# Performance work log

Measured on AMD Instinct MI355X. Metric: run time of the kernel, lower is better.

Reference implementation:

```python
import jax, jax.numpy as jnp
import numpy as np

N = 50000      # nodes
E = 800000     # edges
IN = 128       # in_dim
H = 8          # heads
C = 16         # h_dim (per-head out channels)
ED = 16        # edge_dim
G = 1000       # number of graphs
HC = H * C     # 128
EPS = 1e-16    # PyG softmax epsilon


def setup_inputs() -> dict:
    key = jax.random.key(0)
    ks = jax.random.split(key, 32)
    p = lambda i, shape: jax.random.normal(ks[i], shape, jnp.float32) * 0.1
    inp = {
        "x": jax.random.normal(ks[0], (N, IN), jnp.float32),
        "edge_index": jax.random.randint(ks[1], (2, E), 0, N),
        "edge_attr": jax.random.normal(ks[2], (E, ED), jnp.float32),
        "batch": jnp.sort(jax.random.randint(ks[3], (N,), 0, G)),
    }
    dims = [IN, HC, HC]
    for l in range(3):
        d = dims[l]
        inp[f"W{l+1}"] = p(4 + 6 * l, (d, HC))     # lin weight
        inp[f"We{l+1}"] = p(5 + 6 * l, (ED, HC))   # lin_edge weight
        inp[f"as{l+1}"] = p(6 + 6 * l, (H, C))     # att_src
        inp[f"ad{l+1}"] = p(7 + 6 * l, (H, C))     # att_dst
        inp[f"ae{l+1}"] = p(8 + 6 * l, (H, C))     # att_edge
        inp[f"b{l+1}"] = jnp.zeros((HC,), jnp.float32)
    D = 4 * HC  # cat(h1,h2,h3,h_pool_) -> 512
    inp["Wl1"] = p(22, (D, D)); inp["bl1"] = jnp.zeros((D,), jnp.float32)
    inp["Wl2"] = p(23, (D, 1)); inp["bl2"] = jnp.zeros((1,), jnp.float32)
    return inp


def gat_conv(x, src, dst, edge_attr, W, We, a_s, a_d, a_e, b):
    # x: [N, d_in] -> xs: [N, H, C]
    xs = (x @ W).reshape(-1, H, C)
    ea = (edge_attr @ We).reshape(-1, H, C)          # [E, H, C]
    al_src = jnp.sum(xs * a_s, axis=-1)              # [N, H]
    al_dst = jnp.sum(xs * a_d, axis=-1)              # [N, H]
    al_e = jnp.sum(ea * a_e, axis=-1)                # [E, H]
    alpha = al_src[src] + al_dst[dst] + al_e         # [E, H]
    alpha = jax.nn.leaky_relu(alpha, 0.2)
    amax = jax.ops.segment_max(alpha, dst, num_segments=N)
    ex = jnp.exp(alpha - amax[dst])
    denom = jax.ops.segment_sum(ex, dst, num_segments=N)
    alpha = ex / (denom[dst] + EPS)                  # softmax over in-edges of dst
    msg = xs[src] * alpha[..., None]                 # [E, H, C]
    out = jax.ops.segment_sum(msg, dst, num_segments=N)  # [N, H, C]
    return out.reshape(-1, HC) + b


def reference(x, edge_index, edge_attr, batch,
              W1, We1, as1, ad1, ae1, b1,
              W2, We2, as2, ad2, ae2, b2,
              W3, We3, as3, ad3, ae3, b3,
              Wl1, bl1, Wl2, bl2):
    src, dst = edge_index[0], edge_index[1]
    h1 = gat_conv(x, src, dst, edge_attr, W1, We1, as1, ad1, ae1, b1)
    h2 = gat_conv(h1, src, dst, edge_attr, W2, We2, as2, ad2, ae2, b2)
    h3 = gat_conv(h2, src, dst, edge_attr, W3, We3, as3, ad3, ae3, b3)
    # global_add_pool then broadcast back per node (vectorized gather,
    # replacing the original per-node python loop)
    h_pool = jax.ops.segment_sum(h3, batch, num_segments=G)   # [G, HC]
    h_pool_ = h_pool[batch]                                    # [N, HC]
    h = jnp.concatenate([h1, h2, h3, h_pool_], axis=1)         # [N, 4*HC]
    h = jax.nn.leaky_relu(h @ Wl1 + bl1, 0.01)
    return h @ Wl2 + bl2
```

## Files before the change

kernel.cpp:

```cpp
#include <hip/hip_runtime.h>

#define N_NODES 50000
#define N_EDGES 800000
#define N_GRAPH 1000
#define EPAD (N_EDGES + 8 * N_NODES)

typedef short bf16x8 __attribute__((ext_vector_type(8)));
typedef float f32x4 __attribute__((ext_vector_type(4)));

__device__ inline short f2b(float f) {
    union { float f; unsigned u; } x; x.f = f;
    unsigned r = x.u + 0x7FFF + ((x.u >> 16) & 1);
    return (short)(r >> 16);
}
__device__ inline float b2f_lo(unsigned v) {
    union { unsigned u; float f; } x; x.u = v << 16; return x.f;
}
__device__ inline float b2f_hi(unsigned v) {
    union { unsigned u; float f; } x; x.u = v & 0xFFFF0000u; return x.f;
}
__device__ inline float b2f_s(short s) {
    union { unsigned u; float f; } x; x.u = ((unsigned)(unsigned short)s) << 16; return x.f;
}
__device__ inline unsigned pack2(short lo, short hi) {
    return ((unsigned)(unsigned short)lo) | (((unsigned)(unsigned short)hi) << 16);
}

__global__ void wbt3_k(const float* __restrict__ W0, const float* __restrict__ W1,
                       const float* __restrict__ W2, short* __restrict__ wbt) {
    int l = blockIdx.x >> 6;
    const float* W = (l == 0) ? W0 : (l == 1) ? W1 : W2;
    int idx = (blockIdx.x & 63) * 256 + threadIdx.x;
    int k = idx >> 7, c = idx & 127;
    wbt[(size_t)l * 16384 + (size_t)c * 128 + k] = f2b(W[idx]);
}

__global__ void aew3_k(const float* __restrict__ We0, const float* __restrict__ ae0,
                       const float* __restrict__ We1, const float* __restrict__ ae1,
                       const float* __restrict__ We2, const float* __restrict__ ae2,
                       float* __restrict__ aeW3) {
    const float* We = (blockIdx.x == 0) ? We0 : (blockIdx.x == 1) ? We1 : We2;
    const float* ae = (blockIdx.x == 0) ? ae0 : (blockIdx.x == 1) ? ae1 : ae2;
    int t = threadIdx.x;
    int k = t >> 3, h = t & 7;
    float s = 0.f;
#pragma unroll
    for (int c = 0; c < 16; c++) s += We[k * 128 + h * 16 + c] * ae[h * 16 + c];
    aeW3[blockIdx.x * 128 + t] = s;
}

template <bool AF32>
__global__ __launch_bounds__(256) void gemm_mfma(const void* __restrict__ Aptr,
                                                 const short* __restrict__ WbT,
                                                 short* __restrict__ outb, int nrows) {
    const int tid = threadIdx.x;
    const int n0 = blockIdx.x * 64;
    const int wid = tid >> 6, lane = tid & 63;
    const int lr = lane & 15, kg = lane >> 4;
    const int wr = (wid >> 1) * 32;
    const int wc = (wid & 1) * 64;

    f32x4 acc[2][4] = {};

#pragma unroll
    for (int ks = 0; ks < 4; ks++) {
        const int k0 = ks * 32;
        bf16x8 a[2], b[4];
#pragma unroll
        for (int fm = 0; fm < 2; fm++) {
            int gr = n0 + wr + fm * 16 + lr;
            bf16x8 v = {};
            if (gr < nrows) {
                if (AF32) {
                    const float* ap = (const float*)Aptr + (size_t)gr * 128 + k0 + kg * 8;
                    float4 f0 = *(const float4*)(ap);
                    float4 f1 = *(const float4*)(ap + 4);
                    v[0] = f2b(f0.x); v[1] = f2b(f0.y); v[2] = f2b(f0.z); v[3] = f2b(f0.w);
                    v[4] = f2b(f1.x); v[5] = f2b(f1.y); v[6] = f2b(f1.z); v[7] = f2b(f1.w);
                } else {
                    v = *(const bf16x8*)((const short*)Aptr + (size_t)gr * 128 + k0 + kg * 8);
                }
            }
            a[fm] = v;
        }
#pragma unroll
        for (int fn = 0; fn < 4; fn++)
            b[fn] = *(const bf16x8*)(WbT + (size_t)(wc + fn * 16 + lr) * 128 + k0 + kg * 8);
#pragma unroll
        for (int fm = 0; fm < 2; fm++)
#pragma unroll
            for (int fn = 0; fn < 4; fn++)
                acc[fm][fn] = __builtin_amdgcn_mfma_f32_16x16x32_bf16(
                    a[fm], b[fn], acc[fm][fn], 0, 0, 0);
    }
#pragma unroll
    for (int fm = 0; fm < 2; fm++) {
#pragma unroll
        for (int r = 0; r < 4; r++) {
            int gr = n0 + wr + fm * 16 + kg * 4 + r;
            if (gr < nrows) {
#pragma unroll
                for (int fn = 0; fn < 4; fn++) {
                    int col = wc + fn * 16 + lr;
                    outb[(size_t)gr * 128 + col] = f2b(acc[fm][fn][r]);
                }
            }
        }
    }
}

__global__ void node_al(const short* __restrict__ xsb, const float* __restrict__ a_s,
                        const float* __restrict__ a_d, float* __restrict__ alsrc,
                        float* __restrict__ aldst, int n) {
    int t = blockIdx.x * blockDim.x + threadIdx.x;
    if (t >= n * 8) return;
    int node = t >> 3, h = t & 7;
    const short* xp = xsb + (size_t)node * 128 + h * 16;
    uint4 u0 = *(const uint4*)(xp);
    uint4 u1 = *(const uint4*)(xp + 8);
    unsigned w[8] = {u0.x, u0.y, u0.z, u0.w, u1.x, u1.y, u1.z, u1.w};
    float ss = 0.f, dd = 0.f;
#pragma unroll
    for (int q = 0; q < 8; q++) {
        float lo = b2f_lo(w[q]), hi = b2f_hi(w[q]);
        ss += lo * a_s[h * 16 + q * 2] + hi * a_s[h * 16 + q * 2 + 1];
        dd += lo * a_d[h * 16 + q * 2] + hi * a_d[h * 16 + q * 2 + 1];
    }
    alsrc[t] = ss;
    aldst[t] = dd;
}

__global__ void hist_k(const int* __restrict__ ei, int* __restrict__ cnt, int ne) {
    int e = blockIdx.x * blockDim.x + threadIdx.x;
    if (e < ne) atomicAdd(&cnt[ei[ne + e]], 1);
}

__global__ void scan1_k(const int* __restrict__ cnt, int* __restrict__ rowptr,
                        int* __restrict__ part, int n) {
    __shared__ int s[256];
    int tid = threadIdx.x;
    int i = blockIdx.x * 256 + tid;
    int v = (i < n) ? ((cnt[i] + 7) & ~7) : 0;
    s[tid] = v; __syncthreads();
#pragma unroll
    for (int off = 1; off < 256; off <<= 1) {
        int t = (tid >= off) ? s[tid - off] : 0;
        __syncthreads();
        s[tid] += t;
        __syncthreads();
    }
    if (i < n) rowptr[i] = s[tid] - v;
    if (tid == 255) part[blockIdx.x] = s[255];
}

__global__ void scan2_k(int* __restrict__ part, int npart) {
    __shared__ int s[256];
    int tid = threadIdx.x;
    int v = (tid < npart) ? part[tid] : 0;
    s[tid] = v; __syncthreads();
#pragma unroll
    for (int off = 1; off < 256; off <<= 1) {
        int t = (tid >= off) ? s[tid - off] : 0;
        __syncthreads();
        s[tid] += t;
        __syncthreads();
    }
    if (tid < npart) part[tid] = s[tid] - v;
}

__global__ void scan3_k(int* __restrict__ rowptr, const int* __restrict__ part,
                        const int* __restrict__ cnt, int* __restrict__ cursor, int n) {
    int i = blockIdx.x * 256 + threadIdx.x;
    if (i < n) {
        int r = rowptr[i] + part[blockIdx.x];
        rowptr[i] = r;
        cursor[i] = r;
        if (i == n - 1) rowptr[n] = r + ((cnt[i] + 7) & ~7);
    }
}

__global__ void scatter_k(const int* __restrict__ ei, const float* __restrict__ eattr,
                          int* __restrict__ cursor, int* __restrict__ csr_src,
                          short* __restrict__ eatb, int ne) {
    int e = blockIdx.x * blockDim.x + threadIdx.x;
    if (e >= ne) return;
    int d = ei[ne + e];
    int p = atomicAdd(&cursor[d], 1);
    csr_src[p] = ei[e];
    const float4* ep = (const float4*)(eattr + (size_t)e * 16);
    short* op = eatb + (size_t)p * 16;
#pragma unroll
    for (int q = 0; q < 4; q++) {
        float4 v = ep[q];
        *(short4*)(op + q * 4) = make_short4(f2b(v.x), f2b(v.y), f2b(v.z), f2b(v.w));
    }
}

__global__ void gbound_k(const int* __restrict__ batch, int* __restrict__ gb, int n, int g) {
    int i = blockIdx.x * 256 + threadIdx.x;
    if (i >= n) return;
    int b1 = batch[i];
    int b0 = (i == 0) ? -1 : batch[i - 1];
    for (int q = b0 + 1; q <= b1; q++) gb[q] = i;
    if (i == n - 1)
        for (int q = b1 + 1; q <= g; q++) gb[q] = n;
}

__global__ __launch_bounds__(256) void pools_k(const short* __restrict__ h3b,
                                               const int* __restrict__ gb,
                                               short* __restrict__ poolb) {
    __shared__ float red[128];
    int g = blockIdx.x;
    int c = threadIdx.x & 127;
    int par = threadIdx.x >> 7;
    int i0 = gb[g], i1 = gb[g + 1];
    float s = 0.f;
    for (int i = i0 + par; i < i1; i += 2) s += b2f_s(h3b[(size_t)i * 128 + c]);
    if (par == 1) red[c] = s;
    __syncthreads();
    if (par == 0) poolb[(size_t)g * 128 + c] = f2b(s + red[c]);
}

__global__ __launch_bounds__(256) void gather_k(const int* __restrict__ rowptr,
                                                const int* __restrict__ csr_src,
                                                const short* __restrict__ eatb,
                                                const float* __restrict__ aeW,
                                                const float* __restrict__ alsrc,
                                                const float* __restrict__ aldst,
                                                const short* __restrict__ xsb,
                                                const float* __restrict__ b,
                                                short* __restrict__ houtb, int n) {
    __shared__ float sAe[128];
    if (threadIdx.x < 128) sAe[threadIdx.x] = aeW[threadIdx.x];
    __syncthreads();
    int dst = blockIdx.x * 4 + (threadIdx.x >> 6);
    if (dst >= n) return;
    const int lane = threadIdx.x & 63;
    const int h  = lane >> 3;
    const int pe = lane >> 3;
    const int ph = lane & 7;
    const float L2E = 1.44269504f;
    int p0 = rowptr[dst], p1 = rowptr[dst + 1];
    float ald_p = aldst[dst * 8 + ph];
    float den = 0.f, acc0 = 0.f, acc1 = 0.f;
    const int nfull = (p1 - p0) >> 3;
    int p = p0;
    int svo = 0; unsigned w = 0;
    if (nfull > 0) {
        svo = csr_src[p + pe];
        w = *(const unsigned*)(eatb + (size_t)(p + pe) * 16 + ph * 2);
    }
    for (int c = 0; c < nfull; c++) {
        int csv = svo; unsigned cw = w;
        int pn = p + 8;
        if (c + 1 < nfull) {
            svo = csr_src[pn + pe];
            w = *(const unsigned*)(eatb + (size_t)(pn + pe) * 16 + ph * 2);
        }
        int sc = csv < 0 ? 0 : csv;
        float pal = alsrc[sc * 8 + ph];
#pragma unroll
        for (int k = 0; k < 8; k++) {
            unsigned u = __shfl(cw, pe * 8 + k);
            pal += b2f_lo(u) * sAe[k * 16 + ph] + b2f_hi(u) * sAe[k * 16 + 8 + ph];
        }
        float lg = pal + ald_p;
        lg = lg > 0.f ? lg : 0.2f * lg;
        float pex = exp2f(lg * L2E);
        if (csv < 0) pex = 0.f;
        int t0 = __shfl(csv, 0),  t1 = __shfl(csv, 8),  t2 = __shfl(csv, 16), t3 = __shfl(csv, 24);
        int t4 = __shfl(csv, 32), t5 = __shfl(csv, 40), t6 = __shfl(csv, 48), t7 = __shfl(csv, 56);
        t0 = t0 < 0 ? 0 : t0;  t1 = t1 < 0 ? 0 : t1;
        t2 = t2 < 0 ? 0 : t2;  t3 = t3 < 0 ? 0 : t3;
        t4 = t4 < 0 ? 0 : t4;  t5 = t5 < 0 ? 0 : t5;
        t6 = t6 < 0 ? 0 : t6;  t7 = t7 < 0 ? 0 : t7;
        unsigned v0 = *(const unsigned*)(xsb + (size_t)t0 * 128 + lane * 2);
        unsigned v1 = *(const unsigned*)(xsb + (size_t)t1 * 128 + lane * 2);
        unsigned v2 = *(const unsigned*)(xsb + (size_t)t2 * 128 + lane * 2);
        unsigned v3 = *(const unsigned*)(xsb + (size_t)t3 * 128 + lane * 2);
        unsigned v4 = *(const unsigned*)(xsb + (size_t)t4 * 128 + lane * 2);
        unsigned v5 = *(const unsigned*)(xsb + (size_t)t5 * 128 + lane * 2);
        unsigned v6 = *(const unsigned*)(xsb + (size_t)t6 * 128 + lane * 2);
        unsigned v7 = *(const unsigned*)(xsb + (size_t)t7 * 128 + lane * 2);
        unsigned vv[8] = {v0, v1, v2, v3, v4, v5, v6, v7};
#pragma unroll
        for (int i = 0; i < 8; i++) {
            float ex = __shfl(pex, i * 8 + h);
            den  += ex;
            acc0 += b2f_lo(vv[i]) * ex;
            acc1 += b2f_hi(vv[i]) * ex;
        }
        p = pn;
    }
    float inv = 1.f / (den + 1e-16f);
    const float2 bb = *(const float2*)(b + lane * 2);
    unsigned o = pack2(f2b(acc0 * inv + bb.x), f2b(acc1 * inv + bb.y));
    *(unsigned*)(houtb + (size_t)dst * 128 + lane * 2) = o;
}

__global__ void wl1t_k(const float* __restrict__ Wl1, short* __restrict__ Wl1T) {
    int idx = blockIdx.x * blockDim.x + threadIdx.x;
    int k = idx >> 9, c = idx & 511;
    Wl1T[(size_t)c * 512 + k] = f2b(Wl1[idx]);
}

__global__ void init_out(float* __restrict__ out, const float* __restrict__ bl2, int n) {
    int t = blockIdx.x * blockDim.x + threadIdx.x;
    if (t < n) out[t] = bl2[0];
}

__global__ __launch_bounds__(256) void final_mfma(
    const short* __restrict__ h1, const short* __restrict__ h2,
    const short* __restrict__ h3, const short* __restrict__ poolb,
    const int* __restrict__ batch, const short* __restrict__ Wl1T,
    const float* __restrict__ bl1, const float* __restrict__ Wl2,
    float* __restrict__ out, int nrows)
{
    __shared__ short Abuf[2][16 * 64 * 8];
    __shared__ int   sBatch[64];
    const int tid = threadIdx.x;
    const int n0 = blockIdx.x * 64;
    const int j0 = blockIdx.y * 256;
    const int wid = tid >> 6, lane = tid & 63;
    const int lr = lane & 15, kg = lane >> 4;

    if (tid < 64) {
        int gr = n0 + tid;
        sBatch[tid] = (gr < nrows) ? batch[gr] : 0;
    }
    __syncthreads();

    const short* seg_base[4] = {h1, h2, h3, poolb};

    auto STAGE = [&](int t) {
        const short* base = seg_base[t];
        int gr = n0 + lane;
        int grow = (t == 3) ? sBatch[lane] : ((gr < nrows) ? gr : 0);
        const short* rowp = base + (size_t)grow * 128;
#pragma unroll
        for (int q = 0; q < 4; q++) {
            const short* src = rowp + q * 32 + wid * 8;
#if __has_builtin(__builtin_amdgcn_global_load_lds)
            __builtin_amdgcn_global_load_lds(
                (const __attribute__((address_space(1))) unsigned int*)src,
                (__attribute__((address_space(3))) unsigned int*)
                    &Abuf[t & 1][((q * 4 + wid) * 64 + lane) * 8],
                16, 0, 0);
#else
            uint4 v = *(const uint4*)src;
            *(uint4*)(&Abuf[t & 1][((q * 4 + wid) * 64 + lane) * 8]) = v;
#endif
        }
    };

    f32x4 acc[4][4] = {};

    STAGE(0);
    __syncthreads();
#pragma unroll
    for (int t = 0; t < 4; t++) {
        if (t < 3) STAGE(t + 1);
#pragma unroll
        for (int ks = 0; ks < 4; ks++) {
            bf16x8 a[4], b[4];
#pragma unroll
            for (int fn = 0; fn < 4; fn++)
                b[fn] = *(const bf16x8*)(Wl1T + (size_t)(j0 + wid * 64 + fn * 16 + lr) * 512
                                         + t * 128 + ks * 32 + kg * 8);
#pragma unroll
            for (int fm = 0; fm < 4; fm++)
                a[fm] = *(const bf16x8*)(&Abuf[t & 1][((ks * 4 + kg) * 64 + fm * 16 + lr) * 8]);
#pragma unroll
            for (int fm = 0; fm < 4; fm++)
#pragma unroll
                for (int fn = 0; fn < 4; fn++)
                    acc[fm][fn] = __builtin_amdgcn_mfma_f32_16x16x32_bf16(
                        a[fm], b[fn], acc[fm][fn], 0, 0, 0);
        }
        if (t < 3) __syncthreads();
    }

    float w2[4], b1c[4];
#pragma unroll
    for (int fn = 0; fn < 4; fn++) {
        int c = j0 + wid * 64 + fn * 16 + lr;
        w2[fn]  = Wl2[c];
        b1c[fn] = bl1[c];
    }

#pragma unroll
    for (int fm = 0; fm < 4; fm++) {
#pragma unroll
        for (int r = 0; r < 4; r++) {
            float s = 0.f;
#pragma unroll
            for (int fn = 0; fn < 4; fn++) {
                float z = acc[fm][fn][r] + b1c[fn];
                z = z > 0.f ? z : 0.01f * z;
                s += z * w2[fn];
            }
            s += __shfl_xor(s, 1);
            s += __shfl_xor(s, 2);
            s += __shfl_xor(s, 4);
            s += __shfl_xor(s, 8);
            if (lr == 0) {
                int gr = n0 + fm * 16 + kg * 4 + r;
                if (gr < nrows) atomicAdd(out + gr, s);
            }
        }
    }
}

extern "C" void kernel_launch(void* const* d_in, const int* in_sizes, int n_in,
                              void* d_out, int out_size, void* d_ws, size_t ws_size,
                              hipStream_t stream) {
    const float* x     = (const float*)d_in[0];
    const int*   ei    = (const int*)d_in[1];
    const float* eattr = (const float*)d_in[2];
    const int*   batch = (const int*)d_in[3];
    const float* W[3]   = {(const float*)d_in[4],  (const float*)d_in[10], (const float*)d_in[16]};
    const float* We[3]  = {(const float*)d_in[5],  (const float*)d_in[11], (const float*)d_in[17]};
    const float* as_[3] = {(const float*)d_in[6],  (const float*)d_in[12], (const float*)d_in[18]};
    const float* ad_[3] = {(const float*)d_in[7],  (const float*)d_in[13], (const float*)d_in[19]};
    const float* ae_[3] = {(const float*)d_in[8],  (const float*)d_in[14], (const float*)d_in[20]};
    const float* b_[3]  = {(const float*)d_in[9],  (const float*)d_in[15], (const float*)d_in[21]};
    const float* Wl1 = (const float*)d_in[22];
    const float* bl1 = (const float*)d_in[23];
    const float* Wl2 = (const float*)d_in[24];
    const float* bl2 = (const float*)d_in[25];

    const int N = N_NODES, E = N_EDGES, G = N_GRAPH;

    float* ws    = (float*)d_ws;
    float* alsrc = ws;
    float* aldst = alsrc + (size_t)N * 8;
    float* aeW3  = aldst + (size_t)N * 8;
    short* xsb   = (short*)(aeW3 + 384);
    short* hb0   = xsb + (size_t)N * 128;
    short* hb1   = hb0 + (size_t)N * 128;
    short* hb2   = hb1 + (size_t)N * 128;
    short* hb[3] = {hb0, hb1, hb2};
    short* poolb = hb2 + (size_t)N * 128;
    short* wbt   = poolb + (size_t)G * 128;
    short* wl1t  = wbt + 3 * 16384;
    short* eatb  = wl1t + 262144;
    int*   cnt     = (int*)(eatb + (size_t)EPAD * 16);
    int*   rowptr  = cnt + N;
    int*   cursor  = rowptr + N + 1;
    int*   part    = cursor + N;
    int*   gb      = part + 256;
    int*   csr_src = gb + G + 1;

    wbt3_k<<<192, 256, 0, stream>>>(W[0], W[1], W[2], wbt);
    wl1t_k<<<1024, 256, 0, stream>>>(Wl1, wl1t);
    aew3_k<<<3, 128, 0, stream>>>(We[0], ae_[0], We[1], ae_[1], We[2], ae_[2], aeW3);
    hipMemsetAsync(cnt, 0, (size_t)N * sizeof(int), stream);
    hipMemsetAsync(csr_src, 0x80, (size_t)EPAD * sizeof(int), stream);
    hist_k<<<(E + 255) / 256, 256, 0, stream>>>(ei, cnt, E);
    const int nblk = (N + 255) / 256;
    scan1_k<<<nblk, 256, 0, stream>>>(cnt, rowptr, part, N);
    scan2_k<<<1, 256, 0, stream>>>(part, nblk);
    scan3_k<<<nblk, 256, 0, stream>>>(rowptr, part, cnt, cursor, N);
    scatter_k<<<(E + 255) / 256, 256, 0, stream>>>(ei, eattr, cursor, csr_src, eatb, E);
    gbound_k<<<nblk, 256, 0, stream>>>(batch, gb, N, G);

    for (int l = 0; l < 3; l++) {
        if (l == 0)
            gemm_mfma<true><<<(N + 63) / 64, 256, 0, stream>>>(x, wbt, xsb, N);
        else
            gemm_mfma<false><<<(N + 63) / 64, 256, 0, stream>>>(hb[l - 1], wbt + l * 16384,
                                                                xsb, N);
        node_al<<<(N * 8 + 255) / 256, 256, 0, stream>>>(xsb, as_[l], ad_[l], alsrc, aldst, N);
        gather_k<<<(N + 3) / 4, 256, 0, stream>>>(rowptr, csr_src, eatb, aeW3 + l * 128,
                                                  alsrc, aldst, xsb, b_[l], hb[l], N);
    }
    pools_k<<<G, 256, 0, stream>>>(hb[2], gb, poolb);

    init_out<<<(N + 255) / 256, 256, 0, stream>>>((float*)d_out, bl2, N);
    dim3 fg((N + 63) / 64, 2);
    final_mfma<<<fg, 256, 0, stream>>>(hb[0], hb[1], hb[2], poolb, batch,
                                       wl1t, bl1, Wl2, (float*)d_out, N);
}
```

Before: 402.2 us.

## Split each destination node's edge chunks across two wavefronts and reduce via LDS

```diff
diff --git a/kernel.cpp b/kernel.cpp
--- a/kernel.cpp
+++ b/kernel.cpp
@@ -231,11 +231,13 @@
                                                 const float* __restrict__ b,
                                                 short* __restrict__ houtb, int n) {
     __shared__ float sAe[128];
+    __shared__ float sDen[2][64], sA0[2][64], sA1[2][64];
     if (threadIdx.x < 128) sAe[threadIdx.x] = aeW[threadIdx.x];
     __syncthreads();
-    int dst = blockIdx.x * 4 + (threadIdx.x >> 6);
-    if (dst >= n) return;
+    const int pi   = threadIdx.x >> 7;
+    const int wv   = (threadIdx.x >> 6) & 1;
     const int lane = threadIdx.x & 63;
+    const int dst  = blockIdx.x * 2 + pi;
     const int h  = lane >> 3;
     const int pe = lane >> 3;
     const int ph = lane & 7;
@@ -244,18 +246,19 @@
     float ald_p = aldst[dst * 8 + ph];
     float den = 0.f, acc0 = 0.f, acc1 = 0.f;
     const int nfull = (p1 - p0) >> 3;
-    int p = p0;
+    int c = wv;
     int svo = 0; unsigned w = 0;
-    if (nfull > 0) {
+    if (c < nfull) {
+        int p = p0 + c * 8;
         svo = csr_src[p + pe];
         w = *(const unsigned*)(eatb + (size_t)(p + pe) * 16 + ph * 2);
     }
-    for (int c = 0; c < nfull; c++) {
+    for (; c < nfull; c += 2) {
         int csv = svo; unsigned cw = w;
-        int pn = p + 8;
-        if (c + 1 < nfull) {
-            svo = csr_src[pn + pe];
-            w = *(const unsigned*)(eatb + (size_t)(pn + pe) * 16 + ph * 2);
+        if (c + 2 < nfull) {
+            int pnx = p0 + (c + 2) * 8;
+            svo = csr_src[pnx + pe];
+            w = *(const unsigned*)(eatb + (size_t)(pnx + pe) * 16 + ph * 2);
         }
         int sc = csv < 0 ? 0 : csv;
         float pal = alsrc[sc * 8 + ph];
@@ -290,12 +293,22 @@
             acc0 += b2f_lo(vv[i]) * ex;
             acc1 += b2f_hi(vv[i]) * ex;
         }
-        p = pn;
-    }
-    float inv = 1.f / (den + 1e-16f);
-    const float2 bb = *(const float2*)(b + lane * 2);
-    unsigned o = pack2(f2b(acc0 * inv + bb.x), f2b(acc1 * inv + bb.y));
-    *(unsigned*)(houtb + (size_t)dst * 128 + lane * 2) = o;
+    }
+    if (wv == 1) {
+        sDen[pi][lane] = den;
+        sA0[pi][lane] = acc0;
+        sA1[pi][lane] = acc1;
+    }
+    __syncthreads();
+    if (wv == 0) {
+        den  += sDen[pi][lane];
+        acc0 += sA0[pi][lane];
+        acc1 += sA1[pi][lane];
+        float inv = 1.f / (den + 1e-16f);
+        const float2 bb = *(const float2*)(b + lane * 2);
+        unsigned o = pack2(f2b(acc0 * inv + bb.x), f2b(acc1 * inv + bb.y));
+        *(unsigned*)(houtb + (size_t)dst * 128 + lane * 2) = o;
+    }
 }
 
 __global__ void wl1t_k(const float* __restrict__ Wl1, short* __restrict__ Wl1T) {
@@ -471,8 +484,8 @@
             gemm_mfma<false><<<(N + 63) / 64, 256, 0, stream>>>(hb[l - 1], wbt + l * 16384,
                                                                 xsb, N);
         node_al<<<(N * 8 + 255) / 256, 256, 0, stream>>>(xsb, as_[l], ad_[l], alsrc, aldst, N);
-        gather_k<<<(N + 3) / 4, 256, 0, stream>>>(rowptr, csr_src, eatb, aeW3 + l * 128,
-                                                  alsrc, aldst, xsb, b_[l], hb[l], N);
+        gather_k<<<N / 2, 256, 0, stream>>>(rowptr, csr_src, eatb, aeW3 + l * 128,
+                                            alsrc, aldst, xsb, b_[l], hb[l], N);
     }
     pools_k<<<G, 256, 0, stream>>>(hb[2], gb, poolb);
 
```

Measured after the change: 444.2 us. 1.1x slower.
